# Optimization experiments

Measured on AMD Instinct MI355X. Metric: run time of the kernel, lower is better.

## Reference

```python
import jax, jax.numpy as jnp
import numpy as np

N = 131072   # n_nodes == n_edges (required by the broadcast in the original module)
C = 256      # node_channels == edge_channels (required by the broadcast)
EPS_BN = 1e-5
EPS = 1e-5


def _linear_params(key, out_c, in_c):
    k1, k2 = jax.random.split(key)
    bound = 1.0 / np.sqrt(in_c)
    W = jax.random.uniform(k1, (out_c, in_c), minval=-bound, maxval=bound, dtype=jnp.float32)
    b = jax.random.uniform(k2, (out_c,), minval=-bound, maxval=bound, dtype=jnp.float32)
    return W, b


def setup_inputs() -> dict:
    key = jax.random.key(0)
    ks = jax.random.split(key, 10)
    h = jax.random.normal(ks[0], (N, C), dtype=jnp.float32)
    e = jax.random.normal(ks[1], (N, C), dtype=jnp.float32)
    edge_index = jax.random.randint(ks[2], (2, N), 0, N, dtype=jnp.int64)
    A_w, A_b = _linear_params(ks[3], C, C)
    B_w, B_b = _linear_params(ks[4], C, C)
    C_w, C_b = _linear_params(ks[5], C, C)
    D_w, D_b = _linear_params(ks[6], C, C)
    U_w, U_b = _linear_params(ks[7], C, C)
    V_w, V_b = _linear_params(ks[8], C, C)
    bn_gamma = jnp.ones((C,), dtype=jnp.float32)
    bn_beta = jnp.zeros((C,), dtype=jnp.float32)
    return dict(h=h, edge_index=edge_index, e=e,
                A_w=A_w, A_b=A_b, B_w=B_w, B_b=B_b,
                C_w=C_w, C_b=C_b, D_w=D_w, D_b=D_b,
                bn_gamma=bn_gamma, bn_beta=bn_beta,
                U_w=U_w, U_b=U_b, V_w=V_w, V_b=V_b)


def reference(h, edge_index, e,
              A_w, A_b, B_w, B_b, C_w, C_b, D_w, D_b,
              bn_gamma, bn_beta, U_w, U_b, V_w, V_b):
    row, col = edge_index[0], edge_index[1]
    # gather + four parallel linears, summed: [E, C]
    e_out = (h[row] @ A_w.T + A_b
             + h[col] @ B_w.T + B_b
             + e[col] @ C_w.T + C_b
             + e[row] @ D_w.T + D_b)
    # BatchNorm1d (training mode: batch stats, biased variance) + ReLU
    mu = jnp.mean(e_out, axis=0)
    var = jnp.var(e_out, axis=0)
    e_out = jax.nn.relu(bn_gamma * (e_out - mu) * jax.lax.rsqrt(var + EPS_BN) + bn_beta)
    # scatter-add edge messages into node-indexed e, then sigmoid-normalize over dim 0
    e_new = e.at[row].add(e_out)
    e_new = jax.nn.sigmoid(e_new)
    e_new = e_new / (jnp.sum(e_new, axis=0, keepdims=True) + EPS)
    # final gather-multiply-reduce: (e_new * V(h[col])).sum(0) broadcasts [N,C]*[E,C] with N==E
    h_out = h @ U_w.T + U_b + jnp.sum(e_new * (h[col] @ V_w.T + V_b), axis=0)
    h_out = jax.nn.relu(h_out)
    return h_out, e_new
```

## Files before the change

### kernel.cpp

```cpp
#include <hip/hip_runtime.h>
#include <hip/hip_bf16.h>


typedef __attribute__((ext_vector_type(8))) short bf16x8;
typedef __attribute__((ext_vector_type(4))) float f32x4;

__device__ __forceinline__ float b2f(unsigned int lo16) {
  union { unsigned int u; float f; } c; c.u = lo16 << 16; return c.f;
}
__device__ __forceinline__ float lof(unsigned int u) { return b2f(u & 0xffffu); }
__device__ __forceinline__ float hif(unsigned int u) { return b2f(u >> 16); }
__device__ __forceinline__ unsigned int f2b(float f) {
  union { float f; unsigned int u; } c; c.f = f;
  unsigned int u = c.u;
  u += 0x7fffu + ((u >> 16) & 1u);
  return u >> 16;
}

__device__ __forceinline__ void prep_chunk(const float* __restrict__ src,
                                           unsigned short* __restrict__ dst, int g) {
  int mtile = g >> 9;
  int rem = g & 511;
  int r = rem >> 5, k8 = rem & 31;
  const float4* s = reinterpret_cast<const float4*>(src + (((size_t)mtile * 16 + r) << 8) + k8 * 8);
  float4 v0 = s[0], v1 = s[1];
  uint4 o;
  o.x = f2b(v0.x) | (f2b(v0.y) << 16);
  o.y = f2b(v0.z) | (f2b(v0.w) << 16);
  o.z = f2b(v1.x) | (f2b(v1.y) << 16);
  o.w = f2b(v1.z) | (f2b(v1.w) << 16);
  *reinterpret_cast<uint4*>(dst + ((size_t)mtile * 512 + k8 * 16 + r) * 8) = o;
}

__global__ __launch_bounds__(256) void prep_he(const float* __restrict__ h,
                                               unsigned short* __restrict__ h_t,
                                               const float* __restrict__ e,
                                               unsigned short* __restrict__ e_t,
                                               int nChunksEach) {
  int g = blockIdx.x * 256 + threadIdx.x;
  if (g < nChunksEach) prep_chunk(h, h_t, g);
  else if (g < 2 * nChunksEach) prep_chunk(e, e_t, g - nChunksEach);
}

__global__ __launch_bounds__(256) void prep_weights(
    const float* __restrict__ s0, const float* __restrict__ s1,
    const float* __restrict__ s2, const float* __restrict__ s3,
    const float* __restrict__ s4, const float* __restrict__ s5,
    unsigned short* __restrict__ W1h, unsigned short* __restrict__ W1e,
    unsigned short* __restrict__ W2t) {
  int g = blockIdx.x * 256 + threadIdx.x;
  int sel = g >> 13;
  int gg = g & 8191;
  const float* src; unsigned short* dst;
  switch (sel) {
    case 0: src = s0; dst = W1h; break;
    case 1: src = s1; dst = W1h + 65536; break;
    case 2: src = s2; dst = W1e; break;
    case 3: src = s3; dst = W1e + 65536; break;
    case 4: src = s4; dst = W2t; break;
    default: src = s5; dst = W2t + 65536; break;
  }
  prep_chunk(src, dst, gg);
}

__global__ __launch_bounds__(256) void gemm_bt2(
    const unsigned short* __restrict__ Ah, const unsigned short* __restrict__ Ae,
    const unsigned short* __restrict__ Bh, const unsigned short* __restrict__ Be,
    const float* __restrict__ bias, unsigned short* __restrict__ Cmat,
    int O, int nColBlk, int ktSteps, int nBlk) {
  __shared__ char lds[16384];
  const int cpx = nBlk >> 3;
  const int hw = blockIdx.x;
  const int bid = (hw % 8) * cpx + hw / 8;
  const int colBlk = bid % nColBlk;
  const int rowBlk = bid / nColBlk;
  const int tid = threadIdx.x;
  const int w = tid >> 6, lane = tid & 63;
  const int wm = w >> 1, wn = w & 1;

  const size_t aTileOff = (size_t)(rowBlk * 8 + w * 2) * 8192 + lane * 16;
  const size_t bTileOff = (size_t)(colBlk * 8 + w * 2) * 8192 + lane * 16;
  char* ldsA0 = lds + (w * 2) * 1024;
  char* ldsA1 = lds + (w * 2 + 1) * 1024;
  char* ldsB0 = lds + 8192 + (w * 2) * 1024;
  char* ldsB1 = lds + 8192 + (w * 2 + 1) * 1024;

  f32x4 acc[4][4] = {};

  for (int kt = 0; kt < ktSteps; ++kt) {
    const char* Abase = (const char*)(kt < 8 ? Ah : Ae) + aTileOff + (size_t)(kt & 7) * 1024;
    const char* Bbase = (const char*)(kt < 8 ? Bh : Be) + bTileOff + (size_t)(kt & 7) * 1024;
    __builtin_amdgcn_global_load_lds((const __attribute__((address_space(1))) void*)Abase,
                                     (__attribute__((address_space(3))) void*)ldsA0, 16, 0, 0);
    __builtin_amdgcn_global_load_lds((const __attribute__((address_space(1))) void*)(Abase + 8192),
                                     (__attribute__((address_space(3))) void*)ldsA1, 16, 0, 0);
    __builtin_amdgcn_global_load_lds((const __attribute__((address_space(1))) void*)Bbase,
                                     (__attribute__((address_space(3))) void*)ldsB0, 16, 0, 0);
    __builtin_amdgcn_global_load_lds((const __attribute__((address_space(1))) void*)(Bbase + 8192),
                                     (__attribute__((address_space(3))) void*)ldsB1, 16, 0, 0);
    __syncthreads();
    bf16x8 a[4], b[4];
#pragma unroll
    for (int mi = 0; mi < 4; ++mi)
      a[mi] = *reinterpret_cast<const bf16x8*>(lds + (wm * 4 + mi) * 1024 + lane * 16);
#pragma unroll
    for (int ni = 0; ni < 4; ++ni)
      b[ni] = *reinterpret_cast<const bf16x8*>(lds + 8192 + (wn * 4 + ni) * 1024 + lane * 16);
#pragma unroll
    for (int mi = 0; mi < 4; ++mi)
#pragma unroll
      for (int ni = 0; ni < 4; ++ni)
        acc[mi][ni] = __builtin_amdgcn_mfma_f32_16x16x32_bf16(a[mi], b[ni], acc[mi][ni], 0, 0, 0);
    __syncthreads();
  }

  const int rb = rowBlk * 128 + wm * 64 + ((lane >> 4) << 2);
  const int cb = colBlk * 128 + wn * 64 + (lane & 15);
#pragma unroll
  for (int mi = 0; mi < 4; ++mi) {
#pragma unroll
    for (int ni = 0; ni < 4; ++ni) {
      const int coln = cb + ni * 16;
      const float bz = bias[coln];
      const size_t base = (size_t)(rb + mi * 16) * O + coln;
#pragma unroll
      for (int r = 0; r < 4; ++r)
        Cmat[base + (size_t)r * O] = (unsigned short)f2b(acc[mi][ni][r] + bz);
    }
  }
}

__global__ __launch_bounds__(256) void edge_stats(
    const unsigned short* __restrict__ PRPC,
    const int* __restrict__ rows_s, const int* __restrict__ cols_s,
    float* __restrict__ sums, float* __restrict__ sumsq) {
  __shared__ float red[8][256];
  const int c8 = threadIdx.x & 31;
  const int sub = threadIdx.x >> 5;
  float s[8], q[8];
#pragma unroll
  for (int j = 0; j < 8; ++j) { s[j] = 0.f; q[j] = 0.f; }
#pragma unroll 1
  for (int grp = 0; grp < 2; ++grp) {
    const int kb = blockIdx.x * 64 + grp * 32 + sub * 4;
    int r[4], cj[4];
#pragma unroll
    for (int u = 0; u < 4; ++u) { r[u] = rows_s[kb + u]; cj[u] = cols_s[kb + u]; }
    uint4 pr[4], pc[4];
#pragma unroll
    for (int u = 0; u < 4; ++u)
      pr[u] = *reinterpret_cast<const uint4*>(PRPC + (size_t)r[u] * 512 + c8 * 8);
#pragma unroll
    for (int u = 0; u < 4; ++u)
      pc[u] = *reinterpret_cast<const uint4*>(PRPC + (size_t)cj[u] * 512 + 256 + c8 * 8);
#pragma unroll
    for (int u = 0; u < 4; ++u) {
      const unsigned int rw[4] = {pr[u].x, pr[u].y, pr[u].z, pr[u].w};
      const unsigned int cw[4] = {pc[u].x, pc[u].y, pc[u].z, pc[u].w};
#pragma unroll
      for (int p4 = 0; p4 < 4; ++p4) {
        const float v0 = lof(rw[p4]) + lof(cw[p4]);
        const float v1 = hif(rw[p4]) + hif(cw[p4]);
        s[2 * p4] += v0;     q[2 * p4] += v0 * v0;
        s[2 * p4 + 1] += v1; q[2 * p4 + 1] += v1 * v1;
      }
    }
  }
#pragma unroll
  for (int j = 0; j < 8; ++j) red[sub][c8 * 8 + j] = s[j];
  __syncthreads();
  {
    const int c = threadIdx.x;
    float t = 0.f;
#pragma unroll
    for (int u2 = 0; u2 < 8; ++u2) t += red[u2][c];
    atomicAdd(sums + c, t);
  }
  __syncthreads();
#pragma unroll
  for (int j = 0; j < 8; ++j) red[sub][c8 * 8 + j] = q[j];
  __syncthreads();
  {
    const int c = threadIdx.x;
    float t = 0.f;
#pragma unroll
    for (int u2 = 0; u2 < 8; ++u2) t += red[u2][c];
    atomicAdd(sumsq + c, t);
  }
}

__global__ __launch_bounds__(256) void hist_rows(const int* __restrict__ ei,
                                                 const int* __restrict__ modep,
                                                 int* __restrict__ cnt, int Nn) {
  const int k = blockIdx.x * 256 + threadIdx.x;
  if (k >= Nn) return;
  const int row = (*modep) ? ei[2 * k] : ei[k];
  atomicAdd(&cnt[row], 1);
}

__global__ __launch_bounds__(256) void scan1(const int* __restrict__ cnt,
                                             int* __restrict__ bsum) {
  __shared__ int red[256];
  const int t = threadIdx.x;
  red[t] = cnt[blockIdx.x * 256 + t];
  __syncthreads();
#pragma unroll
  for (int s = 128; s > 0; s >>= 1) {
    if (t < s) red[t] += red[t + s];
    __syncthreads();
  }
  if (t == 0) bsum[blockIdx.x] = red[0];
}

__global__ __launch_bounds__(512) void scan2(int* __restrict__ bsum, int nb) {
  __shared__ int tmp[512];
  const int t = threadIdx.x;
  const int own = (t < nb) ? bsum[t] : 0;
  tmp[t] = own;
  __syncthreads();
  for (int off = 1; off < 512; off <<= 1) {
    int v = (t >= off) ? tmp[t - off] : 0;
    __syncthreads();
    tmp[t] += v;
    __syncthreads();
  }
  if (t < nb) bsum[t] = tmp[t] - own;
}

__global__ __launch_bounds__(256) void scan3(const int* __restrict__ cnt,
                                             const int* __restrict__ bsum,
                                             int* __restrict__ base, int Nn) {
  __shared__ int tmp[256];
  const int t = threadIdx.x;
  const int gid = blockIdx.x * 256 + t;
  const int own = cnt[gid];
  tmp[t] = own;
  __syncthreads();
  for (int off = 1; off < 256; off <<= 1) {
    int v = (t >= off) ? tmp[t - off] : 0;
    __syncthreads();
    tmp[t] += v;
    __syncthreads();
  }
  base[gid] = tmp[t] - own + bsum[blockIdx.x];
  if (gid == 0) base[Nn] = Nn;
}

__global__ __launch_bounds__(256) void scatter_eids(const int* __restrict__ ei,
                                                    const int* __restrict__ modep,
                                                    const int* __restrict__ base,
                                                    int* __restrict__ cnt,
                                                    int* __restrict__ rows_s,
                                                    int* __restrict__ cols_s, int Nn) {
  const int k = blockIdx.x * 256 + threadIdx.x;
  if (k >= Nn) return;
  int row, col;
  if (*modep) { row = ei[2 * k]; col = ei[2 * (Nn + k)]; }
  else        { row = ei[k];     col = ei[Nn + k]; }
  const int pos = base[row] + atomicAdd(&cnt[row], -1) - 1;
  rows_s[pos] = row;
  cols_s[pos] = col;
}

#define GCAP 1024
__global__ __launch_bounds__(256) void gather_sig_colsum(
    const float* __restrict__ e, const unsigned short* __restrict__ PRPC,
    const int* __restrict__ base, const int* __restrict__ cols_s,
    const float* __restrict__ sums, const float* __restrict__ sumsq,
    const float* __restrict__ gamma, const float* __restrict__ beta,
    float* __restrict__ acc, float* __restrict__ colsum, float invE) {
  __shared__ float red[4][256];
  __shared__ int colsL[GCAP];
  __shared__ int baseL[65];
  const int lane = threadIdx.x & 63, w = threadIdx.x >> 6;
  const int n0 = blockIdx.x * 64;
  if (threadIdx.x < 65) baseL[threadIdx.x] = base[n0 + threadIdx.x];
  __syncthreads();
  const int bstart = baseL[0];
  const int bcount = baseL[64] - bstart;
  for (int qq = threadIdx.x; qq < bcount && qq < GCAP; qq += 256)
    colsL[qq] = cols_s[bstart + qq];
  const float4 sm = *reinterpret_cast<const float4*>(sums + lane * 4);
  const float4 sq = *reinterpret_cast<const float4*>(sumsq + lane * 4);
  const float4 gm = *reinterpret_cast<const float4*>(gamma + lane * 4);
  const float4 bt = *reinterpret_cast<const float4*>(beta + lane * 4);
  float4 sc, sh;
  {
    const float mx = sm.x * invE, my = sm.y * invE, mz = sm.z * invE, mw = sm.w * invE;
    sc.x = gm.x * rsqrtf(fmaxf(sq.x * invE - mx * mx, 0.f) + 1e-5f);
    sc.y = gm.y * rsqrtf(fmaxf(sq.y * invE - my * my, 0.f) + 1e-5f);
    sc.z = gm.z * rsqrtf(fmaxf(sq.z * invE - mz * mz, 0.f) + 1e-5f);
    sc.w = gm.w * rsqrtf(fmaxf(sq.w * invE - mw * mw, 0.f) + 1e-5f);
    sh.x = bt.x - mx * sc.x; sh.y = bt.y - my * sc.y;
    sh.z = bt.z - mz * sc.z; sh.w = bt.w - mw * sc.w;
  }
  __syncthreads();
  float s0 = 0.f, s1 = 0.f, s2 = 0.f, s3 = 0.f;
  const int i0 = n0 + w * 16;
  int p = baseL[w * 16];
  const int pendW = baseL[w * 16 + 16];
  uint2 pcn;
  pcn.x = 0; pcn.y = 0;
  if (p < pendW) {
    const int q0 = p - bstart;
    const int cj = (q0 < GCAP) ? colsL[q0] : cols_s[p];
    pcn = *reinterpret_cast<const uint2*>(PRPC + (size_t)cj * 512 + 256 + lane * 4);
  }
  float4 ev = *reinterpret_cast<const float4*>(e + (size_t)i0 * 256 + lane * 4);
  uint2 prv = *reinterpret_cast<const uint2*>(PRPC + (size_t)i0 * 512 + lane * 4);
#pragma unroll 1
  for (int it = 0; it < 16; ++it) {
    float4 v = ev;
    const uint2 pr = prv;
    if (it + 1 < 16) {
      ev = *reinterpret_cast<const float4*>(e + (size_t)(i0 + it + 1) * 256 + lane * 4);
      prv = *reinterpret_cast<const uint2*>(PRPC + (size_t)(i0 + it + 1) * 512 + lane * 4);
    }
    const float pr0 = lof(pr.x), pr1 = hif(pr.x), pr2 = lof(pr.y), pr3 = hif(pr.y);
    const int pe = baseL[w * 16 + it + 1];
#pragma unroll 1
    while (p < pe) {
      const uint2 pc = pcn;
      if (p + 1 < pendW) {
        const int qn = p + 1 - bstart;
        const int cj = (qn < GCAP) ? colsL[qn] : cols_s[p + 1];
        pcn = *reinterpret_cast<const uint2*>(PRPC + (size_t)cj * 512 + 256 + lane * 4);
      }
      v.x += fmaxf(fmaf(sc.x, pr0 + lof(pc.x), sh.x), 0.f);
      v.y += fmaxf(fmaf(sc.y, pr1 + hif(pc.x), sh.y), 0.f);
      v.z += fmaxf(fmaf(sc.z, pr2 + lof(pc.y), sh.z), 0.f);
      v.w += fmaxf(fmaf(sc.w, pr3 + hif(pc.y), sh.w), 0.f);
      ++p;
    }
    v.x = 1.f / (1.f + __expf(-v.x));
    v.y = 1.f / (1.f + __expf(-v.y));
    v.z = 1.f / (1.f + __expf(-v.z));
    v.w = 1.f / (1.f + __expf(-v.w));
    *reinterpret_cast<float4*>(acc + (size_t)(i0 + it) * 256 + lane * 4) = v;
    s0 += v.x; s1 += v.y; s2 += v.z; s3 += v.w;
  }
  red[w][lane * 4 + 0] = s0;
  red[w][lane * 4 + 1] = s1;
  red[w][lane * 4 + 2] = s2;
  red[w][lane * 4 + 3] = s3;
  __syncthreads();
  const int c = threadIdx.x;
  atomicAdd(colsum + c, red[0][c] + red[1][c] + red[2][c] + red[3][c]);
}

__global__ __launch_bounds__(256) void enew_T(
    const float* __restrict__ acc, const float* __restrict__ colsum,
    const int* __restrict__ ei, const int* __restrict__ modep,
    const unsigned short* __restrict__ VU,
    float* __restrict__ outE, float* __restrict__ T, int Nn) {
  __shared__ float red[8][256];
  const int c8 = threadIdx.x & 31, sub = threadIdx.x >> 5;
  const int mode = *modep;
  float iv[8];
#pragma unroll
  for (int j = 0; j < 8; ++j) iv[j] = 1.0f / (colsum[c8 * 8 + j] + 1e-5f);
  float t[8];
#pragma unroll
  for (int j = 0; j < 8; ++j) t[j] = 0.f;
#pragma unroll 1
  for (int grp = 0; grp < 2; ++grp) {
    const int kb = blockIdx.x * 64 + grp * 32 + sub * 4;
    int col[4];
#pragma unroll
    for (int u = 0; u < 4; ++u)
      col[u] = mode ? ei[2 * (Nn + kb + u)] : ei[Nn + kb + u];
    uint4 hv[4];
#pragma unroll
    for (int u = 0; u < 4; ++u)
      hv[u] = *reinterpret_cast<const uint4*>(VU + (size_t)col[u] * 512 + c8 * 8);
    float4 a[4], b[4];
#pragma unroll
    for (int u = 0; u < 4; ++u) {
      const float4* p0 = reinterpret_cast<const float4*>(acc + (size_t)(kb + u) * 256 + c8 * 8);
      a[u] = p0[0]; b[u] = p0[1];
    }
#pragma unroll
    for (int u = 0; u < 4; ++u) {
      float en[8] = {a[u].x * iv[0], a[u].y * iv[1], a[u].z * iv[2], a[u].w * iv[3],
                     b[u].x * iv[4], b[u].y * iv[5], b[u].z * iv[6], b[u].w * iv[7]};
      float4 o0, o1;
      o0.x = en[0]; o0.y = en[1]; o0.z = en[2]; o0.w = en[3];
      o1.x = en[4]; o1.y = en[5]; o1.z = en[6]; o1.w = en[7];
      float4* q0 = reinterpret_cast<float4*>(outE + (size_t)(kb + u) * 256 + c8 * 8);
      q0[0] = o0; q0[1] = o1;
      const unsigned int w4[4] = {hv[u].x, hv[u].y, hv[u].z, hv[u].w};
#pragma unroll
      for (int p = 0; p < 4; ++p) {
        t[2 * p] += en[2 * p] * lof(w4[p]);
        t[2 * p + 1] += en[2 * p + 1] * hif(w4[p]);
      }
    }
  }
#pragma unroll
  for (int j = 0; j < 8; ++j) red[sub][c8 * 8 + j] = t[j];
  __syncthreads();
  {
    const int c = threadIdx.x;
    float tt = 0.f;
#pragma unroll
    for (int u2 = 0; u2 < 8; ++u2) tt += red[u2][c];
    atomicAdd(T + c, tt);
  }
}

__global__ __launch_bounds__(256) void hout_k(
    const unsigned short* __restrict__ VU, const float* __restrict__ T,
    float* __restrict__ outH, int nChunks) {
  const int g = blockIdx.x * 256 + threadIdx.x;
  if (g >= nChunks) return;
  const int i = g >> 5, c8 = g & 31;
  const uint4 hu = *reinterpret_cast<const uint4*>(VU + (size_t)i * 512 + 256 + c8 * 8);
  const float4 t0 = *reinterpret_cast<const float4*>(T + c8 * 8);
  const float4 t1 = *reinterpret_cast<const float4*>(T + c8 * 8 + 4);
  float4 o0, o1;
  o0.x = fmaxf(lof(hu.x) + t0.x, 0.f);
  o0.y = fmaxf(hif(hu.x) + t0.y, 0.f);
  o0.z = fmaxf(lof(hu.y) + t0.z, 0.f);
  o0.w = fmaxf(hif(hu.y) + t0.w, 0.f);
  o1.x = fmaxf(lof(hu.z) + t1.x, 0.f);
  o1.y = fmaxf(hif(hu.z) + t1.y, 0.f);
  o1.z = fmaxf(lof(hu.w) + t1.z, 0.f);
  o1.w = fmaxf(hif(hu.w) + t1.w, 0.f);
  float4* q = reinterpret_cast<float4*>(outH + (size_t)i * 256 + c8 * 8);
  q[0] = o0; q[1] = o1;
}

__global__ void pack_bias2(const float* a, const float* d, const float* b, const float* cc,
                           const float* v, const float* u,
                           float* b1, float* b2) {
  const int t = threadIdx.x;
  b1[t] = a[t] + d[t];
  b1[256 + t] = b[t] + cc[t];
  b2[t] = v[t];
  b2[256 + t] = u[t];
}

__global__ void detect_idx(const int* __restrict__ ei, int* __restrict__ mode) {
  if (threadIdx.x == 0 && blockIdx.x == 0) {
    int m = 0;
#pragma unroll
    for (int i = 1; i < 64; i += 2) m |= ei[i];
    *mode = (m == 0) ? 1 : 0;
  }
}

extern "C" void kernel_launch(void* const* d_in, const int* in_sizes, int n_in,
                              void* d_out, int out_size, void* d_ws, size_t ws_size,
                              hipStream_t stream) {
  const float* h     = (const float*)d_in[0];
  const int*   ei    = (const int*)d_in[1];
  const float* e     = (const float*)d_in[2];
  const float* Aw    = (const float*)d_in[3];
  const float* Ab    = (const float*)d_in[4];
  const float* Bw    = (const float*)d_in[5];
  const float* Bb    = (const float*)d_in[6];
  const float* Cw    = (const float*)d_in[7];
  const float* Cb    = (const float*)d_in[8];
  const float* Dw    = (const float*)d_in[9];
  const float* Db    = (const float*)d_in[10];
  const float* gamma = (const float*)d_in[11];
  const float* beta  = (const float*)d_in[12];
  const float* Uw    = (const float*)d_in[13];
  const float* Ub    = (const float*)d_in[14];
  const float* Vw    = (const float*)d_in[15];
  const float* Vb    = (const float*)d_in[16];
  const int N = in_sizes[0] / 256;

  char* ws = (char*)d_ws;
  unsigned short* W1h = (unsigned short*)(ws + 0x0);
  unsigned short* W1e = (unsigned short*)(ws + 0x40000);
  unsigned short* W2t = (unsigned short*)(ws + 0x80000);
  float* b1     = (float*)(ws + 0xC0000);
  float* b2     = (float*)(ws + 0xC0800);
  float* sums   = (float*)(ws + 0xC1000);
  float* sumsq  = (float*)(ws + 0xC1400);
  float* colsum = (float*)(ws + 0xC1800);
  float* Tacc   = (float*)(ws + 0xC1C00);
  int*   mode   = (int*)(ws + 0xC2C00);
  unsigned short* h_t  = (unsigned short*)(ws + 0x100000);
  unsigned short* e_t  = (unsigned short*)(ws + 0x4100000);
  unsigned short* PRPC = (unsigned short*)(ws + 0x8100000);
  unsigned short* VU   = (unsigned short*)(ws + 0x10100000);
  float*          acc  = (float*)(ws + 0x100000);
  int* cnt    = (int*)(ws + 0x18100000);
  int* baseA  = (int*)(ws + 0x18180000);
  int* rows_s = (int*)(ws + 0x18210000);
  int* cols_s = (int*)(ws + 0x18290000);
  int* bsum   = (int*)(ws + 0x18310000);

  float* outH = (float*)d_out;
  float* outE = outH + (size_t)N * 256;

  hipMemsetAsync(ws + 0xC1000, 0, 4096, stream);
  hipMemsetAsync(cnt, 0, (size_t)N * 4, stream);
  detect_idx<<<1, 64, 0, stream>>>(ei, mode);
  pack_bias2<<<1, 256, 0, stream>>>(Ab, Db, Bb, Cb, Vb, Ub, b1, b2);
  prep_weights<<<192, 256, 0, stream>>>(Aw, Bw, Dw, Cw, Vw, Uw, W1h, W1e, W2t);

  hist_rows<<<N / 256, 256, 0, stream>>>(ei, mode, cnt, N);
  scan1<<<N / 256, 256, 0, stream>>>(cnt, bsum);
  scan2<<<1, 512, 0, stream>>>(bsum, N / 256);
  scan3<<<N / 256, 256, 0, stream>>>(cnt, bsum, baseA, N);
  scatter_eids<<<N / 256, 256, 0, stream>>>(ei, mode, baseA, cnt, rows_s, cols_s, N);

  const int nChunks = N * 32;
  prep_he<<<2 * nChunks / 256, 256, 0, stream>>>(h, h_t, e, e_t, nChunks);
  gemm_bt2<<<(N / 128) * 4, 256, 0, stream>>>(h_t, e_t, W1h, W1e, b1, PRPC, 512, 4, 16, (N / 128) * 4);
  gemm_bt2<<<(N / 128) * 4, 256, 0, stream>>>(h_t, h_t, W2t, W2t, b2, VU, 512, 4, 8, (N / 128) * 4);

  edge_stats<<<N / 64, 256, 0, stream>>>(PRPC, rows_s, cols_s, sums, sumsq);
  gather_sig_colsum<<<N / 64, 256, 0, stream>>>(e, PRPC, baseA, cols_s, sums, sumsq,
                                                gamma, beta, acc, colsum, 1.0f / (float)N);
  enew_T<<<N / 64, 256, 0, stream>>>(acc, colsum, ei, mode, VU, outE, Tacc, N);
  hout_k<<<nChunks / 256, 256, 0, stream>>>(VU, Tacc, outH, nChunks);
}
```

Before: 607.4 us.

## Fuse T reduction into gather kernel using unnormalized sigmoid, merge finalize kernels

The per-column normalization is a constant scale, so sum(e_new*V) equals the raw sigmoid-weighted sum divided by colsum. The gather kernel now accumulates that raw T product in the same pass and stores the sigmoid values as bf16 instead of fp32. A single finalize kernel then writes both outE and outH, replacing the separate enew_T and hout_k kernels, and the bias-pack and index-detect kernels are folded into prep_weights. This saves launches and an fp32 round trip of the intermediate, at the cost of bf16 rounding in the stored e_new values.

```diff
diff --git a/kernel.cpp b/kernel.cpp
--- a/kernel.cpp
+++ b/kernel.cpp
@@ -47,8 +47,26 @@
     const float* __restrict__ s2, const float* __restrict__ s3,
     const float* __restrict__ s4, const float* __restrict__ s5,
     unsigned short* __restrict__ W1h, unsigned short* __restrict__ W1e,
-    unsigned short* __restrict__ W2t) {
+    unsigned short* __restrict__ W2t,
+    const float* __restrict__ Ab, const float* __restrict__ Db,
+    const float* __restrict__ Bb, const float* __restrict__ Cb,
+    const float* __restrict__ Vb, const float* __restrict__ Ub,
+    float* __restrict__ b1, float* __restrict__ b2,
+    const int* __restrict__ ei, int* __restrict__ mode) {
   int g = blockIdx.x * 256 + threadIdx.x;
+  if (blockIdx.x == 0) {
+    const int t = threadIdx.x;
+    b1[t] = Ab[t] + Db[t];
+    b1[256 + t] = Bb[t] + Cb[t];
+    b2[t] = Vb[t];
+    b2[256 + t] = Ub[t];
+    if (t == 0) {
+      int m = 0;
+#pragma unroll
+      for (int i = 1; i < 64; i += 2) m |= ei[i];
+      *mode = (m == 0) ? 1 : 0;
+    }
+  }
   int sel = g >> 13;
   int gg = g & 8191;
   const float* src; unsigned short* dst;
@@ -263,12 +281,15 @@
 }
 
 #define GCAP 1024
-__global__ __launch_bounds__(256) void gather_sig_colsum(
+__global__ __launch_bounds__(256) void gather_sig_T(
     const float* __restrict__ e, const unsigned short* __restrict__ PRPC,
     const int* __restrict__ base, const int* __restrict__ cols_s,
+    const int* __restrict__ ei, const int* __restrict__ modep,
+    const unsigned short* __restrict__ VU,
     const float* __restrict__ sums, const float* __restrict__ sumsq,
     const float* __restrict__ gamma, const float* __restrict__ beta,
-    float* __restrict__ acc, float* __restrict__ colsum, float invE) {
+    unsigned short* __restrict__ accB, float* __restrict__ colsum,
+    float* __restrict__ Traw, float invE, int Nn) {
   __shared__ float red[4][256];
   __shared__ int colsL[GCAP];
   __shared__ int baseL[65];
@@ -295,12 +316,13 @@
     sh.z = bt.z - mz * sc.z; sh.w = bt.w - mw * sc.w;
   }
   __syncthreads();
+  const int mode = *modep;
   float s0 = 0.f, s1 = 0.f, s2 = 0.f, s3 = 0.f;
+  float t0 = 0.f, t1 = 0.f, t2 = 0.f, t3 = 0.f;
   const int i0 = n0 + w * 16;
   int p = baseL[w * 16];
   const int pendW = baseL[w * 16 + 16];
-  uint2 pcn;
-  pcn.x = 0; pcn.y = 0;
+  uint2 pcn; pcn.x = 0; pcn.y = 0;
   if (p < pendW) {
     const int q0 = p - bstart;
     const int cj = (q0 < GCAP) ? colsL[q0] : cols_s[p];
@@ -310,11 +332,14 @@
   uint2 prv = *reinterpret_cast<const uint2*>(PRPC + (size_t)i0 * 512 + lane * 4);
 #pragma unroll 1
   for (int it = 0; it < 16; ++it) {
+    const int i = i0 + it;
+    const int colT = mode ? ei[2 * (Nn + i)] : ei[Nn + i];
+    const uint2 hv = *reinterpret_cast<const uint2*>(VU + (size_t)colT * 512 + lane * 4);
     float4 v = ev;
     const uint2 pr = prv;
     if (it + 1 < 16) {
-      ev = *reinterpret_cast<const float4*>(e + (size_t)(i0 + it + 1) * 256 + lane * 4);
-      prv = *reinterpret_cast<const uint2*>(PRPC + (size_t)(i0 + it + 1) * 512 + lane * 4);
+      ev = *reinterpret_cast<const float4*>(e + (size_t)(i + 1) * 256 + lane * 4);
+      prv = *reinterpret_cast<const uint2*>(PRPC + (size_t)(i + 1) * 512 + lane * 4);
     }
     const float pr0 = lof(pr.x), pr1 = hif(pr.x), pr2 = lof(pr.y), pr3 = hif(pr.y);
     const int pe = baseL[w * 16 + it + 1];
@@ -336,117 +361,73 @@
     v.y = 1.f / (1.f + __expf(-v.y));
     v.z = 1.f / (1.f + __expf(-v.z));
     v.w = 1.f / (1.f + __expf(-v.w));
-    *reinterpret_cast<float4*>(acc + (size_t)(i0 + it) * 256 + lane * 4) = v;
+    uint2 ob;
+    ob.x = f2b(v.x) | (f2b(v.y) << 16);
+    ob.y = f2b(v.z) | (f2b(v.w) << 16);
+    *reinterpret_cast<uint2*>(accB + (size_t)i * 256 + lane * 4) = ob;
     s0 += v.x; s1 += v.y; s2 += v.z; s3 += v.w;
+    t0 += v.x * lof(hv.x); t1 += v.y * hif(hv.x);
+    t2 += v.z * lof(hv.y); t3 += v.w * hif(hv.y);
   }
   red[w][lane * 4 + 0] = s0;
   red[w][lane * 4 + 1] = s1;
   red[w][lane * 4 + 2] = s2;
   red[w][lane * 4 + 3] = s3;
   __syncthreads();
-  const int c = threadIdx.x;
-  atomicAdd(colsum + c, red[0][c] + red[1][c] + red[2][c] + red[3][c]);
-}
-
-__global__ __launch_bounds__(256) void enew_T(
-    const float* __restrict__ acc, const float* __restrict__ colsum,
-    const int* __restrict__ ei, const int* __restrict__ modep,
-    const unsigned short* __restrict__ VU,
-    float* __restrict__ outE, float* __restrict__ T, int Nn) {
-  __shared__ float red[8][256];
-  const int c8 = threadIdx.x & 31, sub = threadIdx.x >> 5;
-  const int mode = *modep;
-  float iv[8];
-#pragma unroll
-  for (int j = 0; j < 8; ++j) iv[j] = 1.0f / (colsum[c8 * 8 + j] + 1e-5f);
-  float t[8];
-#pragma unroll
-  for (int j = 0; j < 8; ++j) t[j] = 0.f;
-#pragma unroll 1
-  for (int grp = 0; grp < 2; ++grp) {
-    const int kb = blockIdx.x * 64 + grp * 32 + sub * 4;
-    int col[4];
-#pragma unroll
-    for (int u = 0; u < 4; ++u)
-      col[u] = mode ? ei[2 * (Nn + kb + u)] : ei[Nn + kb + u];
-    uint4 hv[4];
-#pragma unroll
-    for (int u = 0; u < 4; ++u)
-      hv[u] = *reinterpret_cast<const uint4*>(VU + (size_t)col[u] * 512 + c8 * 8);
-    float4 a[4], b[4];
-#pragma unroll
-    for (int u = 0; u < 4; ++u) {
-      const float4* p0 = reinterpret_cast<const float4*>(acc + (size_t)(kb + u) * 256 + c8 * 8);
-      a[u] = p0[0]; b[u] = p0[1];
-    }
-#pragma unroll
-    for (int u = 0; u < 4; ++u) {
-      float en[8] = {a[u].x * iv[0], a[u].y * iv[1], a[u].z * iv[2], a[u].w * iv[3],
-                     b[u].x * iv[4], b[u].y * iv[5], b[u].z * iv[6], b[u].w * iv[7]};
-      float4 o0, o1;
-      o0.x = en[0]; o0.y = en[1]; o0.z = en[2]; o0.w = en[3];
-      o1.x = en[4]; o1.y = en[5]; o1.z = en[6]; o1.w = en[7];
-      float4* q0 = reinterpret_cast<float4*>(outE + (size_t)(kb + u) * 256 + c8 * 8);
-      q0[0] = o0; q0[1] = o1;
-      const unsigned int w4[4] = {hv[u].x, hv[u].y, hv[u].z, hv[u].w};
-#pragma unroll
-      for (int p = 0; p < 4; ++p) {
-        t[2 * p] += en[2 * p] * lof(w4[p]);
-        t[2 * p + 1] += en[2 * p + 1] * hif(w4[p]);
-      }
-    }
-  }
-#pragma unroll
-  for (int j = 0; j < 8; ++j) red[sub][c8 * 8 + j] = t[j];
-  __syncthreads();
   {
     const int c = threadIdx.x;
-    float tt = 0.f;
-#pragma unroll
-    for (int u2 = 0; u2 < 8; ++u2) tt += red[u2][c];
-    atomicAdd(T + c, tt);
-  }
-}
-
-__global__ __launch_bounds__(256) void hout_k(
-    const unsigned short* __restrict__ VU, const float* __restrict__ T,
-    float* __restrict__ outH, int nChunks) {
+    atomicAdd(colsum + c, red[0][c] + red[1][c] + red[2][c] + red[3][c]);
+  }
+  __syncthreads();
+  red[w][lane * 4 + 0] = t0;
+  red[w][lane * 4 + 1] = t1;
+  red[w][lane * 4 + 2] = t2;
+  red[w][lane * 4 + 3] = t3;
+  __syncthreads();
+  {
+    const int c = threadIdx.x;
+    atomicAdd(Traw + c, red[0][c] + red[1][c] + red[2][c] + red[3][c]);
+  }
+}
+
+__global__ __launch_bounds__(256) void finalize(
+    const unsigned short* __restrict__ accB, const unsigned short* __restrict__ VU,
+    const float* __restrict__ colsum, const float* __restrict__ Traw,
+    float* __restrict__ outE, float* __restrict__ outH, int nChunks) {
   const int g = blockIdx.x * 256 + threadIdx.x;
   if (g >= nChunks) return;
   const int i = g >> 5, c8 = g & 31;
+  const float4 cs0 = *reinterpret_cast<const float4*>(colsum + c8 * 8);
+  const float4 cs1 = *reinterpret_cast<const float4*>(colsum + c8 * 8 + 4);
+  const float4 tr0 = *reinterpret_cast<const float4*>(Traw + c8 * 8);
+  const float4 tr1 = *reinterpret_cast<const float4*>(Traw + c8 * 8 + 4);
+  float iv[8] = {1.f / (cs0.x + 1e-5f), 1.f / (cs0.y + 1e-5f),
+                 1.f / (cs0.z + 1e-5f), 1.f / (cs0.w + 1e-5f),
+                 1.f / (cs1.x + 1e-5f), 1.f / (cs1.y + 1e-5f),
+                 1.f / (cs1.z + 1e-5f), 1.f / (cs1.w + 1e-5f)};
+  float tt[8] = {tr0.x * iv[0], tr0.y * iv[1], tr0.z * iv[2], tr0.w * iv[3],
+                 tr1.x * iv[4], tr1.y * iv[5], tr1.z * iv[6], tr1.w * iv[7]};
+  const uint4 sb = *reinterpret_cast<const uint4*>(accB + (size_t)i * 256 + c8 * 8);
+  const unsigned int sw[4] = {sb.x, sb.y, sb.z, sb.w};
+  float4 e0, e1;
+  e0.x = lof(sw[0]) * iv[0]; e0.y = hif(sw[0]) * iv[1];
+  e0.z = lof(sw[1]) * iv[2]; e0.w = hif(sw[1]) * iv[3];
+  e1.x = lof(sw[2]) * iv[4]; e1.y = hif(sw[2]) * iv[5];
+  e1.z = lof(sw[3]) * iv[6]; e1.w = hif(sw[3]) * iv[7];
+  float4* qe = reinterpret_cast<float4*>(outE + (size_t)i * 256 + c8 * 8);
+  qe[0] = e0; qe[1] = e1;
   const uint4 hu = *reinterpret_cast<const uint4*>(VU + (size_t)i * 512 + 256 + c8 * 8);
-  const float4 t0 = *reinterpret_cast<const float4*>(T + c8 * 8);
-  const float4 t1 = *reinterpret_cast<const float4*>(T + c8 * 8 + 4);
   float4 o0, o1;
-  o0.x = fmaxf(lof(hu.x) + t0.x, 0.f);
-  o0.y = fmaxf(hif(hu.x) + t0.y, 0.f);
-  o0.z = fmaxf(lof(hu.y) + t0.z, 0.f);
-  o0.w = fmaxf(hif(hu.y) + t0.w, 0.f);
-  o1.x = fmaxf(lof(hu.z) + t1.x, 0.f);
-  o1.y = fmaxf(hif(hu.z) + t1.y, 0.f);
-  o1.z = fmaxf(lof(hu.w) + t1.z, 0.f);
-  o1.w = fmaxf(hif(hu.w) + t1.w, 0.f);
-  float4* q = reinterpret_cast<float4*>(outH + (size_t)i * 256 + c8 * 8);
-  q[0] = o0; q[1] = o1;
-}
-
-__global__ void pack_bias2(const float* a, const float* d, const float* b, const float* cc,
-                           const float* v, const float* u,
-                           float* b1, float* b2) {
-  const int t = threadIdx.x;
-  b1[t] = a[t] + d[t];
-  b1[256 + t] = b[t] + cc[t];
-  b2[t] = v[t];
-  b2[256 + t] = u[t];
-}
-
-__global__ void detect_idx(const int* __restrict__ ei, int* __restrict__ mode) {
-  if (threadIdx.x == 0 && blockIdx.x == 0) {
-    int m = 0;
-#pragma unroll
-    for (int i = 1; i < 64; i += 2) m |= ei[i];
-    *mode = (m == 0) ? 1 : 0;
-  }
+  o0.x = fmaxf(lof(hu.x) + tt[0], 0.f);
+  o0.y = fmaxf(hif(hu.x) + tt[1], 0.f);
+  o0.z = fmaxf(lof(hu.y) + tt[2], 0.f);
+  o0.w = fmaxf(hif(hu.y) + tt[3], 0.f);
+  o1.x = fmaxf(lof(hu.z) + tt[4], 0.f);
+  o1.y = fmaxf(hif(hu.z) + tt[5], 0.f);
+  o1.z = fmaxf(lof(hu.w) + tt[6], 0.f);
+  o1.w = fmaxf(hif(hu.w) + tt[7], 0.f);
+  float4* qh = reinterpret_cast<float4*>(outH + (size_t)i * 256 + c8 * 8);
+  qh[0] = o0; qh[1] = o1;
 }
 
 extern "C" void kernel_launch(void* const* d_in, const int* in_sizes, int n_in,
@@ -480,13 +461,13 @@
   float* sums   = (float*)(ws + 0xC1000);
   float* sumsq  = (float*)(ws + 0xC1400);
   float* colsum = (float*)(ws + 0xC1800);
-  float* Tacc   = (float*)(ws + 0xC1C00);
+  float* Traw   = (float*)(ws + 0xC1C00);
   int*   mode   = (int*)(ws + 0xC2C00);
   unsigned short* h_t  = (unsigned short*)(ws + 0x100000);
   unsigned short* e_t  = (unsigned short*)(ws + 0x4100000);
   unsigned short* PRPC = (unsigned short*)(ws + 0x8100000);
   unsigned short* VU   = (unsigned short*)(ws + 0x10100000);
-  float*          acc  = (float*)(ws + 0x100000);
+  unsigned short* accB = (unsigned short*)(ws + 0x100000);
   int* cnt    = (int*)(ws + 0x18100000);
   int* baseA  = (int*)(ws + 0x18180000);
   int* rows_s = (int*)(ws + 0x18210000);
@@ -498,9 +479,8 @@
 
   hipMemsetAsync(ws + 0xC1000, 0, 4096, stream);
   hipMemsetAsync(cnt, 0, (size_t)N * 4, stream);
-  detect_idx<<<1, 64, 0, stream>>>(ei, mode);
-  pack_bias2<<<1, 256, 0, stream>>>(Ab, Db, Bb, Cb, Vb, Ub, b1, b2);
-  prep_weights<<<192, 256, 0, stream>>>(Aw, Bw, Dw, Cw, Vw, Uw, W1h, W1e, W2t);
+  prep_weights<<<192, 256, 0, stream>>>(Aw, Bw, Dw, Cw, Vw, Uw, W1h, W1e, W2t,
+                                        Ab, Db, Bb, Cb, Vb, Ub, b1, b2, ei, mode);
 
   hist_rows<<<N / 256, 256, 0, stream>>>(ei, mode, cnt, N);
   scan1<<<N / 256, 256, 0, stream>>>(cnt, bsum);
@@ -514,8 +494,8 @@
   gemm_bt2<<<(N / 128) * 4, 256, 0, stream>>>(h_t, h_t, W2t, W2t, b2, VU, 512, 4, 8, (N / 128) * 4);
 
   edge_stats<<<N / 64, 256, 0, stream>>>(PRPC, rows_s, cols_s, sums, sumsq);
-  gather_sig_colsum<<<N / 64, 256, 0, stream>>>(e, PRPC, baseA, cols_s, sums, sumsq,
-                                                gamma, beta, acc, colsum, 1.0f / (float)N);
-  enew_T<<<N / 64, 256, 0, stream>>>(acc, colsum, ei, mode, VU, outE, Tacc, N);
-  hout_k<<<nChunks / 256, 256, 0, stream>>>(VU, Tacc, outH, nChunks);
-}
+  gather_sig_T<<<N / 64, 256, 0, stream>>>(e, PRPC, baseA, cols_s, ei, mode, VU,
+                                           sums, sumsq, gamma, beta,
+                                           accB, colsum, Traw, 1.0f / (float)N, N);
+  finalize<<<nChunks / 256, 256, 0, stream>>>(accB, VU, colsum, Traw, outE, outH, nChunks);
+}
```

Measured after the change: 574.1 us. -5.5%, faster.
